# Optimization experiments

Measured on AMD Instinct MI355X. Metric: run time of the kernel, lower is better.

## Reference

```python
import jax, jax.numpy as jnp
import numpy as np

D_MODEL = 2048
NUM_HEADS = 16
D_K = D_MODEL // NUM_HEADS
THETA = 10000.0
BATCH, SEQ = 2, 2048


def setup_inputs() -> dict:
    key = jax.random.key(0)
    ks = jax.random.split(key, 5)
    scale = 1.0 / np.sqrt(D_MODEL)
    x = jax.random.normal(ks[0], (BATCH, SEQ, D_MODEL), dtype=jnp.float32)
    token_positions = jnp.broadcast_to(jnp.arange(SEQ, dtype=jnp.int32)[None, :], (BATCH, SEQ))
    Wq = jax.random.normal(ks[1], (D_MODEL, D_MODEL), dtype=jnp.float32) * scale
    Wk = jax.random.normal(ks[2], (D_MODEL, D_MODEL), dtype=jnp.float32) * scale
    Wv = jax.random.normal(ks[3], (D_MODEL, D_MODEL), dtype=jnp.float32) * scale
    Wo = jax.random.normal(ks[4], (D_MODEL, D_MODEL), dtype=jnp.float32) * scale
    return {"x": x, "token_positions": token_positions, "Wq": Wq, "Wk": Wk, "Wv": Wv, "Wo": Wo}


def _apply_rope(t, positions):
    # t: [b, h, s, d_k]; positions: [b, s]. Interleaved-pair rotation.
    half = D_K // 2
    inv_freq = THETA ** (-jnp.arange(0, half, dtype=jnp.float32) * 2.0 / D_K)  # [half]
    ang = positions.astype(jnp.float32)[:, :, None] * inv_freq[None, None, :]  # [b, s, half]
    cos = jnp.cos(ang)[:, None, :, :]  # [b, 1, s, half]
    sin = jnp.sin(ang)[:, None, :, :]
    t2 = t.reshape(*t.shape[:-1], half, 2)
    x1, x2 = t2[..., 0], t2[..., 1]
    r1 = x1 * cos - x2 * sin
    r2 = x1 * sin + x2 * cos
    return jnp.stack([r1, r2], axis=-1).reshape(t.shape)


def reference(x, token_positions, Wq, Wk, Wv, Wo):
    b, s, _ = x.shape
    # Linear layers compute x @ W^T (weight stored as [out, in], no bias)
    def proj(w):
        y = jnp.einsum('bsd,ed->bse', x, w)
        return y.reshape(b, s, NUM_HEADS, D_K).transpose(0, 2, 1, 3)  # b h s d
    Q, K, V = proj(Wq), proj(Wk), proj(Wv)
    Q = _apply_rope(Q, token_positions)
    K = _apply_rope(K, token_positions)
    scores = jnp.einsum('bhqd,bhkd->bhqk', Q, K) / jnp.sqrt(jnp.float32(D_K))
    causal = jnp.tril(jnp.ones((s, s), dtype=bool))
    scores = jnp.where(causal[None, None], scores, jnp.finfo(scores.dtype).min)
    attn = jax.nn.softmax(scores, axis=-1)
    out = jnp.einsum('bhqk,bhkd->bhqd', attn, V)  # b h s d
    out = out.transpose(0, 2, 1, 3).reshape(b, s, D_MODEL)
    return jnp.einsum('bse,de->bsd', out, Wo)
```

## Files before the change

kernel.cpp:

```cpp
#include <hip/hip_runtime.h>
#include <cstdint>
#include <cstddef>

#define D_MODEL 2048
#define NHEAD 16
#define DK 128
#define SEQ 2048
#define BATCH 2
#define NTOK (BATCH * SEQ)
#define NQB 32

typedef __bf16 bf16;
typedef __bf16 bf16x2 __attribute__((ext_vector_type(2)));
typedef __bf16 bf16x4 __attribute__((ext_vector_type(4)));
typedef __bf16 bf16x8 __attribute__((ext_vector_type(8)));
typedef float f32x4 __attribute__((ext_vector_type(4)));

__device__ __forceinline__ void g2lds16(const void* g, void* l) {
  __builtin_amdgcn_global_load_lds(
      (const __attribute__((address_space(1))) void*)g,
      (__attribute__((address_space(3))) void*)l, 16, 0, 0);
}

__device__ __forceinline__ void cstore(float* p, float v) { *p = v; }
__device__ __forceinline__ void cstore(bf16* p, float v) { *p = (bf16)v; }

#define BAR()                              \
  {                                        \
    asm volatile("" ::: "memory");         \
    __builtin_amdgcn_s_barrier();          \
    asm volatile("" ::: "memory");         \
  }

__global__ void k_f32_to_bf16(const float* __restrict__ in, bf16* __restrict__ out, int n4) {
  int i = blockIdx.x * blockDim.x + threadIdx.x;
  if (i >= n4) return;
  const float4 v = ((const float4*)in)[i];
  bf16x4 o = {(bf16)v.x, (bf16)v.y, (bf16)v.z, (bf16)v.w};
  ((bf16x4*)out)[i] = o;
}

__global__ void k_w4_to_bf16(const float* __restrict__ W0, const float* __restrict__ W1,
                             const float* __restrict__ W2, const float* __restrict__ W3,
                             bf16* __restrict__ o0, bf16* __restrict__ o1,
                             bf16* __restrict__ o2, bf16* __restrict__ o3, int n4) {
  const float* in;
  bf16* out;
  switch (blockIdx.y) {
    case 0: in = W0; out = o0; break;
    case 1: in = W1; out = o1; break;
    case 2: in = W2; out = o2; break;
    default: in = W3; out = o3;
  }
  int i = blockIdx.x * blockDim.x + threadIdx.x;
  if (i >= n4) return;
  const float4 v = ((const float4*)in)[i];
  bf16x4 o = {(bf16)v.x, (bf16)v.y, (bf16)v.z, (bf16)v.w};
  ((bf16x4*)out)[i] = o;
}

__global__ __launch_bounds__(512, 1) void k_gemm8(
    const bf16* __restrict__ A, const bf16* __restrict__ B0p, const bf16* __restrict__ B1p,
    const bf16* __restrict__ B2p, bf16* __restrict__ C0, bf16* __restrict__ C1,
    bf16* __restrict__ C2, const int* __restrict__ pos, int M, int N, int K) {
  const bf16* Bp = B0p;
  bf16* Cp = C0;
  if (blockIdx.z == 1) { Bp = B1p; Cp = C1; }
  else if (blockIdx.z == 2) { Bp = B2p; Cp = C2; }
  const bool rope = (blockIdx.z < 2);

  __shared__ bf16 Ab[2][256 * 64];
  __shared__ bf16 Bb[2][256 * 64];

  const int t = threadIdx.x;
  const int wid = t >> 6, lane = t & 63;
  const int wr = wid >> 2, wc = wid & 3;
  const int lr = lane & 15, lg = lane >> 4;
  const int bm = blockIdx.y, bn = blockIdx.x;
  const size_t arow0 = (size_t)bm * 256;
  const size_t brow0 = (size_t)bn * 256;

  const int srow = wid * 8 + (lane >> 3);
  const int schunk = ((lane & 7) ^ ((lane >> 3) & 7)) * 8;

#define STG(X, row0, k0, lb, h)                                                \
  {                                                                            \
    g2lds16(&(X)[((row0) + (h)*128 + srow) * (size_t)K + (k0) + schunk],       \
            &(lb)[((h)*128 + wid * 8) * 64]);                                  \
    g2lds16(&(X)[((row0) + (h)*128 + 64 + srow) * (size_t)K + (k0) + schunk],  \
            &(lb)[((h)*128 + 64 + wid * 8) * 64]);                             \
  }
#define LDA8(lb, mh, m, kk) \
  (*(const bf16x8*)&(lb)[((mh)*128 + wr * 64 + (m)*16 + lr) * 64 + ((((kk)*4 + lg) ^ (lr & 7)) * 8)])
#define LDB8(lb, nh, n, kk) \
  (*(const bf16x8*)&(lb)[((nh)*128 + wc * 32 + (n)*16 + lr) * 64 + ((((kk)*4 + lg) ^ (lr & 7)) * 8)])

  const int T = K >> 6;

  STG(A, arow0, 0, Ab[0], 0);
  STG(A, arow0, 0, Ab[0], 1);
  STG(Bp, brow0, 0, Bb[0], 0);
  STG(Bp, brow0, 0, Bb[0], 1);
  STG(A, arow0, 64, Ab[1], 0);

  f32x4 acc[2][2][4][2] = {};

  for (int tt = 0; tt < T; ++tt) {
    const int cur = tt & 1;
    const bf16* Ac = Ab[cur];
    const bf16* Bc = Bb[cur];
    bf16* Aw = Ab[cur];
    bf16* An = Ab[cur ^ 1];
    bf16* Bn = Bb[cur ^ 1];
    const int k1 = (tt + 1) << 6;
    const int k2 = (tt + 2) << 6;
    const bool pf1 = (tt + 1 < T);
    const bool pf2 = (tt + 2 < T);

    if (tt == T - 1) {
      asm volatile("s_waitcnt vmcnt(0)" ::: "memory");
    } else {
      asm volatile("s_waitcnt vmcnt(2)" ::: "memory");
    }
    BAR();

    bf16x8 a[4][2], b0[2][2], b1[2][2];

#pragma unroll
    for (int m = 0; m < 4; ++m)
#pragma unroll
      for (int kk = 0; kk < 2; ++kk) a[m][kk] = LDA8(Ac, 0, m, kk);
#pragma unroll
    for (int n = 0; n < 2; ++n)
#pragma unroll
      for (int kk = 0; kk < 2; ++kk) b0[n][kk] = LDB8(Bc, 0, n, kk);
    if (pf1) {
      STG(A, arow0, k1, An, 1);
      STG(Bp, brow0, k1, Bn, 0);
    }
    __builtin_amdgcn_s_setprio(1);
#pragma unroll
    for (int m = 0; m < 4; ++m)
#pragma unroll
      for (int n = 0; n < 2; ++n)
#pragma unroll
        for (int kk = 0; kk < 2; ++kk)
          acc[0][0][m][n] =
              __builtin_amdgcn_mfma_f32_16x16x32_bf16(a[m][kk], b0[n][kk], acc[0][0][m][n], 0, 0, 0);
    __builtin_amdgcn_s_setprio(0);
    BAR();

#pragma unroll
    for (int n = 0; n < 2; ++n)
#pragma unroll
      for (int kk = 0; kk < 2; ++kk) b1[n][kk] = LDB8(Bc, 1, n, kk);
    if (pf1) STG(Bp, brow0, k1, Bn, 1);
    __builtin_amdgcn_s_setprio(1);
#pragma unroll
    for (int m = 0; m < 4; ++m)
#pragma unroll
      for (int n = 0; n < 2; ++n)
#pragma unroll
        for (int kk = 0; kk < 2; ++kk)
          acc[0][1][m][n] =
              __builtin_amdgcn_mfma_f32_16x16x32_bf16(a[m][kk], b1[n][kk], acc[0][1][m][n], 0, 0, 0);
    __builtin_amdgcn_s_setprio(0);
    BAR();

#pragma unroll
    for (int m = 0; m < 4; ++m)
#pragma unroll
      for (int kk = 0; kk < 2; ++kk) a[m][kk] = LDA8(Ac, 1, m, kk);
    if (pf2) STG(A, arow0, k2, Aw, 0);
    __builtin_amdgcn_s_setprio(1);
#pragma unroll
    for (int m = 0; m < 4; ++m)
#pragma unroll
      for (int n = 0; n < 2; ++n)
#pragma unroll
        for (int kk = 0; kk < 2; ++kk)
          acc[1][1][m][n] =
              __builtin_amdgcn_mfma_f32_16x16x32_bf16(a[m][kk], b1[n][kk], acc[1][1][m][n], 0, 0, 0);
    __builtin_amdgcn_s_setprio(0);
    BAR();

    __builtin_amdgcn_s_setprio(1);
#pragma unroll
    for (int m = 0; m < 4; ++m)
#pragma unroll
      for (int n = 0; n < 2; ++n)
#pragma unroll
        for (int kk = 0; kk < 2; ++kk)
          acc[1][0][m][n] =
              __builtin_amdgcn_mfma_f32_16x16x32_bf16(a[m][kk], b0[n][kk], acc[1][0][m][n], 0, 0, 0);
    __builtin_amdgcn_s_setprio(0);
  }

  float invf[2];
#pragma unroll
  for (int n = 0; n < 2; ++n) {
    int f = ((wc * 32 + n * 16 + lr) & 127) >> 1;
    invf[n] = exp2f((float)f * -0.20762050593121503f);
  }
#pragma unroll
  for (int mh = 0; mh < 2; ++mh)
#pragma unroll
    for (int m = 0; m < 4; ++m) {
      size_t rowb = arow0 + mh * 128 + wr * 64 + m * 16 + lg * 4;
#pragma unroll
      for (int r = 0; r < 4; ++r) {
        float p = rope ? (float)pos[rowb + r] : 0.0f;
#pragma unroll
        for (int n = 0; n < 2; ++n) {
          float sn, cs;
          if (rope) __sincosf(p * invf[n], &sn, &cs);
#pragma unroll
          for (int nh = 0; nh < 2; ++nh) {
            float v = acc[mh][nh][m][n][r];
            float vp = __shfl_xor(v, 1);
            float outv = v;
            if (rope) outv = (lr & 1) ? (v * cs + vp * sn) : (v * cs - vp * sn);
            size_t col = brow0 + nh * 128 + wc * 32 + n * 16 + lr;
            Cp[(rowb + r) * N + col] = (bf16)outv;
          }
        }
      }
    }
#undef STG
#undef LDA8
#undef LDB8
}

template <typename OutT>
__global__ __launch_bounds__(256, 2) void k_gemm_nt(
    const bf16* __restrict__ A, const bf16* __restrict__ B0, const bf16* __restrict__ B1,
    const bf16* __restrict__ B2, OutT* __restrict__ C0, OutT* __restrict__ C1,
    OutT* __restrict__ C2, int M, int N, int K) {
  const bf16* Bp = B0;
  OutT* Cp = C0;
  if (blockIdx.z == 1) { Bp = B1; Cp = C1; }
  else if (blockIdx.z == 2) { Bp = B2; Cp = C2; }

  __shared__ bf16 As[128 * 32];
  __shared__ bf16 Bs[128 * 32];

  const int t = threadIdx.x;
  const int w = t >> 6;
  const int lane = t & 63;
  const int lr = lane & 15;
  const int lg = lane >> 4;
  const int wr = w >> 1, wc = w & 1;
  const int bm = blockIdx.y, bn = blockIdx.x;

  f32x4 acc[4][4] = {};

  const int srow = lane >> 2;
  const int scol = (lane & 3) * 8;

  const int kt_iters = K >> 5;
  for (int kt = 0; kt < kt_iters; ++kt) {
    const int kbase = kt * 32;
#pragma unroll
    for (int i = 0; i < 2; ++i) {
      int chunk = w * 2 + i;
      int row = chunk * 16 + srow;
      g2lds16(&A[(size_t)(bm * 128 + row) * K + kbase + scol], &As[chunk * 512]);
      g2lds16(&Bp[(size_t)(bn * 128 + row) * K + kbase + scol], &Bs[chunk * 512]);
    }
    asm volatile("s_waitcnt vmcnt(0)" ::: "memory");
    __syncthreads();

    bf16x8 af[4], bfr[4];
#pragma unroll
    for (int m = 0; m < 4; ++m)
      af[m] = *(const bf16x8*)&As[(wr * 64 + m * 16 + lr) * 32 + lg * 8];
#pragma unroll
    for (int n = 0; n < 4; ++n)
      bfr[n] = *(const bf16x8*)&Bs[(wc * 64 + n * 16 + lr) * 32 + lg * 8];
#pragma unroll
    for (int m = 0; m < 4; ++m)
#pragma unroll
      for (int n = 0; n < 4; ++n)
        acc[m][n] = __builtin_amdgcn_mfma_f32_16x16x32_bf16(af[m], bfr[n], acc[m][n], 0, 0, 0);
    __syncthreads();
  }

#pragma unroll
  for (int m = 0; m < 4; ++m) {
    int rowb = bm * 128 + wr * 64 + m * 16 + lg * 4;
#pragma unroll
    for (int n = 0; n < 4; ++n) {
      int col = bn * 128 + wc * 64 + n * 16 + lr;
#pragma unroll
      for (int r = 0; r < 4; ++r) cstore(&Cp[(size_t)(rowb + r) * N + col], acc[m][n][r]);
    }
  }
}

__global__ __launch_bounds__(256, 2) void k_attn(const bf16* __restrict__ Q,
                                                 const bf16* __restrict__ K,
                                                 const bf16* __restrict__ V,
                                                 bf16* __restrict__ O) {
  const int wg = blockIdx.x;
  const int g = wg & 7;
  const int i = wg >> 3;
  const int bh = g + 8 * (i & 3);
  const int pr = i >> 2;
  const int b = bh >> 4, h = bh & 15;

  const int t = threadIdx.x;
  const int w = t >> 6, lane = t & 63;
  const int lr = lane & 15, lg = lane >> 4;

  const size_t rowbase = (size_t)b * SEQ;
  const int hoff = h * DK;

  __shared__ bf16 Ks[2][64 * 128];
  __shared__ uint32_t VTu[2][128 * 32];
  __shared__ bf16 Pb[4][16 * 64];

  const int kp = t & 31;
  const int d0s = (t >> 5) * 16;

  const float scale = 0.08838834764831845f;
  const float FIXM = 8.0f;

  bf16x8 sa0, sa1, sb0, sb1;
  int cur = 0;

  const int krow_l = lane >> 4;
  const int kchunk = lane & 15;

  for (int qsel = 0; qsel < 2; ++qsel) {
    const int qblk = qsel ? pr : (NQB - 1 - pr);
    const int qb = qblk * 64;
    const int ktiles = qblk + 1;

    bf16x8 qf[4];
    {
      size_t qrow = rowbase + qb + w * 16 + lr;
#pragma unroll
      for (int c = 0; c < 4; ++c)
        qf[c] = *(const bf16x8*)&Q[qrow * D_MODEL + hoff + c * 32 + lg * 8];
    }

    f32x4 o[8] = {};
    f32x4 lrow = {};

#pragma unroll
    for (int j = 0; j < 4; ++j) {
      int row = w * 16 + j * 4 + krow_l;
      int chunk = kchunk ^ (j * 4 + krow_l);
      g2lds16(&K[(rowbase + row) * D_MODEL + hoff + chunk * 8],
              &Ks[cur][(size_t)(w * 16 + j * 4) * 128]);
    }
    {
      const bf16* vp0 = &V[(rowbase + 2 * kp) * D_MODEL + hoff + d0s];
      sa0 = *(const bf16x8*)vp0;
      sa1 = *(const bf16x8*)(vp0 + 8);
      sb0 = *(const bf16x8*)(vp0 + D_MODEL);
      sb1 = *(const bf16x8*)(vp0 + D_MODEL + 8);
    }

    for (int kt = 0; kt < ktiles; ++kt) {
      const int k0 = kt * 64;
#pragma unroll
      for (int j = 0; j < 8; ++j) {
        int d = d0s + j;
        bf16x2 p0 = {sa0[j], sb0[j]};
        VTu[cur][d * 32 + (kp ^ ((d & 7) << 2))] = *(const uint32_t*)&p0;
      }
#pragma unroll
      for (int j = 0; j < 8; ++j) {
        int d = d0s + 8 + j;
        bf16x2 p1 = {sa1[j], sb1[j]};
        VTu[cur][d * 32 + (kp ^ ((d & 7) << 2))] = *(const uint32_t*)&p1;
      }
      asm volatile("s_waitcnt vmcnt(0)" ::: "memory");
      __syncthreads();

      if (kt + 1 < ktiles) {
#pragma unroll
        for (int j = 0; j < 4; ++j) {
          int row = w * 16 + j * 4 + krow_l;
          int chunk = kchunk ^ (j * 4 + krow_l);
          g2lds16(&K[(rowbase + k0 + 64 + row) * D_MODEL + hoff + chunk * 8],
                  &Ks[cur ^ 1][(size_t)(w * 16 + j * 4) * 128]);
        }
        const bf16* vp0 = &V[(rowbase + k0 + 64 + 2 * kp) * D_MODEL + hoff + d0s];
        sa0 = *(const bf16x8*)vp0;
        sa1 = *(const bf16x8*)(vp0 + 8);
        sb0 = *(const bf16x8*)(vp0 + D_MODEL);
        sb1 = *(const bf16x8*)(vp0 + D_MODEL + 8);
      }

      f32x4 sc[4];
      __builtin_amdgcn_s_setprio(1);
#pragma unroll
      for (int tt = 0; tt < 4; ++tt) {
        f32x4 a = {};
#pragma unroll
        for (int c = 0; c < 4; ++c) {
          bf16x8 kf = *(const bf16x8*)&Ks[cur][(tt * 16 + lr) * 128 + (((c * 4 + lg) ^ lr) * 8)];
          a = __builtin_amdgcn_mfma_f32_16x16x32_bf16(qf[c], kf, a, 0, 0, 0);
        }
        sc[tt] = a * scale;
      }
      __builtin_amdgcn_s_setprio(0);

      const int qrow0 = qb + w * 16 + lg * 4;
      if (k0 + 64 > qb + w * 16) {
#pragma unroll
        for (int tt = 0; tt < 4; ++tt) {
          int kcol = k0 + tt * 16 + lr;
#pragma unroll
          for (int r = 0; r < 4; ++r)
            if (kcol > qrow0 + r) sc[tt][r] = -3.0e38f;
        }
      }

#pragma unroll
      for (int tt = 0; tt < 4; ++tt)
#pragma unroll
        for (int r = 0; r < 4; ++r) {
          float p = __expf(sc[tt][r] - FIXM);
          sc[tt][r] = p;
          lrow[r] += p;
        }

#pragma unroll
      for (int tt = 0; tt < 4; ++tt)
#pragma unroll
        for (int r = 0; r < 4; ++r) {
          int q = lg * 4 + r;
          int col = tt * 16 + lr;
          Pb[w][q * 64 + (col ^ ((q & 7) << 3))] = (bf16)sc[tt][r];
        }
      asm volatile("s_waitcnt lgkmcnt(0)" ::: "memory");
      bf16x8 pf0 = *(const bf16x8*)&Pb[w][lr * 64 + ((lg * 8) ^ ((lr & 7) << 3))];
      bf16x8 pf1 = *(const bf16x8*)&Pb[w][lr * 64 + ((32 + lg * 8) ^ ((lr & 7) << 3))];

      __builtin_amdgcn_s_setprio(1);
#pragma unroll
      for (int nt = 0; nt < 8; ++nt) {
        int d = nt * 16 + lr;
        bf16x8 vf0 = *(const bf16x8*)&VTu[cur][d * 32 + ((lg * 4) ^ ((d & 7) << 2))];
        bf16x8 vf1 = *(const bf16x8*)&VTu[cur][d * 32 + ((16 + lg * 4) ^ ((d & 7) << 2))];
        o[nt] = __builtin_amdgcn_mfma_f32_16x16x32_bf16(pf0, vf0, o[nt], 0, 0, 0);
        o[nt] = __builtin_amdgcn_mfma_f32_16x16x32_bf16(pf1, vf1, o[nt], 0, 0, 0);
      }
      __builtin_amdgcn_s_setprio(0);
      cur ^= 1;
    }

#pragma unroll
    for (int off = 8; off >= 1; off >>= 1)
#pragma unroll
      for (int r = 0; r < 4; ++r) lrow[r] += __shfl_xor(lrow[r], off);

    size_t orow = rowbase + qb + w * 16 + lg * 4;
#pragma unroll
    for (int nt = 0; nt < 8; ++nt)
#pragma unroll
      for (int r = 0; r < 4; ++r)
        O[(orow + r) * D_MODEL + hoff + nt * 16 + lr] = (bf16)(o[nt][r] / lrow[r]);
  }
}

extern "C" void kernel_launch(void* const* d_in, const int* in_sizes, int n_in, void* d_out,
                              int out_size, void* d_ws, size_t ws_size, hipStream_t stream) {
  const float* x = (const float*)d_in[0];
  const int* pos = (const int*)d_in[1];
  const float* Wq = (const float*)d_in[2];
  const float* Wk = (const float*)d_in[3];
  const float* Wv = (const float*)d_in[4];
  const float* Wo = (const float*)d_in[5];
  float* out = (float*)d_out;

  char* ws = (char*)d_ws;
  const size_t MB = 1u << 20;
  bf16* xb  = (bf16*)(ws);
  bf16* wqb = (bf16*)(ws + 16 * MB);
  bf16* wkb = (bf16*)(ws + 24 * MB);
  bf16* wvb = (bf16*)(ws + 32 * MB);
  bf16* wob = (bf16*)(ws + 40 * MB);
  bf16* Qb  = (bf16*)(ws + 48 * MB);
  bf16* Kb  = (bf16*)(ws + 64 * MB);
  bf16* Vb  = (bf16*)(ws + 80 * MB);
  bf16* AOb = (bf16*)(ws + 96 * MB);

  {
    int n4 = NTOK * D_MODEL / 4;
    k_f32_to_bf16<<<(n4 + 255) / 256, 256, 0, stream>>>(x, xb, n4);
    int w4 = D_MODEL * D_MODEL / 4;
    k_w4_to_bf16<<<dim3((w4 + 255) / 256, 4), 256, 0, stream>>>(
        Wq, Wk, Wv, Wo, wqb, wkb, wvb, wob, w4);
  }
  {
    dim3 g(D_MODEL / 256, NTOK / 256, 3);
    k_gemm8<<<g, 512, 0, stream>>>(xb, wqb, wkb, wvb, Qb, Kb, Vb, pos,
                                   NTOK, D_MODEL, D_MODEL);
  }
  k_attn<<<dim3(NQB * NHEAD * BATCH / 2, 1, 1), 256, 0, stream>>>(Qb, Kb, Vb, AOb);
  {
    dim3 g(D_MODEL / 128, NTOK / 128, 1);
    k_gemm_nt<float><<<g, 256, 0, stream>>>(AOb, wob, wob, wob, out, out, out, NTOK, D_MODEL, D_MODEL);
  }
}
```

Measured before the change: 262.5 us.

## Use 128-row query blocks with 8 waves in attention and merge conversion launches

The attention kernel now processes 128 query rows per block with 512 threads (8 waves), instead of 64 rows with 4 waves. Each K/V tile staged in shared memory is therefore reused by twice as many query rows, and the grid shrinks to 256 blocks. Each thread now loads half as much V data per tile. Separately, the x and weight fp32-to-bf16 conversions are merged into one 5-way launch to save a kernel launch, though the weight slices launch extra blocks that exit immediately. Fewer, larger attention blocks may reduce occupancy and worsen the balance of the causal workload.

```diff
diff --git a/kernel.cpp b/kernel.cpp
--- a/kernel.cpp
+++ b/kernel.cpp
@@ -8,7 +8,6 @@
 #define SEQ 2048
 #define BATCH 2
 #define NTOK (BATCH * SEQ)
-#define NQB 32
 
 typedef __bf16 bf16;
 typedef __bf16 bf16x2 __attribute__((ext_vector_type(2)));
@@ -32,28 +31,24 @@
     asm volatile("" ::: "memory");         \
   }
 
-__global__ void k_f32_to_bf16(const float* __restrict__ in, bf16* __restrict__ out, int n4) {
-  int i = blockIdx.x * blockDim.x + threadIdx.x;
-  if (i >= n4) return;
-  const float4 v = ((const float4*)in)[i];
-  bf16x4 o = {(bf16)v.x, (bf16)v.y, (bf16)v.z, (bf16)v.w};
-  ((bf16x4*)out)[i] = o;
-}
-
-__global__ void k_w4_to_bf16(const float* __restrict__ W0, const float* __restrict__ W1,
-                             const float* __restrict__ W2, const float* __restrict__ W3,
-                             bf16* __restrict__ o0, bf16* __restrict__ o1,
-                             bf16* __restrict__ o2, bf16* __restrict__ o3, int n4) {
+__global__ void k_conv5(const float* __restrict__ X, const float* __restrict__ W0,
+                        const float* __restrict__ W1, const float* __restrict__ W2,
+                        const float* __restrict__ W3, bf16* __restrict__ xo,
+                        bf16* __restrict__ o0, bf16* __restrict__ o1,
+                        bf16* __restrict__ o2, bf16* __restrict__ o3,
+                        int nx4, int nw4) {
   const float* in;
   bf16* out;
+  int n;
   switch (blockIdx.y) {
-    case 0: in = W0; out = o0; break;
-    case 1: in = W1; out = o1; break;
-    case 2: in = W2; out = o2; break;
-    default: in = W3; out = o3;
+    case 0: in = X; out = xo; n = nx4; break;
+    case 1: in = W0; out = o0; n = nw4; break;
+    case 2: in = W1; out = o1; n = nw4; break;
+    case 3: in = W2; out = o2; n = nw4; break;
+    default: in = W3; out = o3; n = nw4;
   }
   int i = blockIdx.x * blockDim.x + threadIdx.x;
-  if (i >= n4) return;
+  if (i >= n) return;
   const float4 v = ((const float4*)in)[i];
   bf16x4 o = {(bf16)v.x, (bf16)v.y, (bf16)v.z, (bf16)v.w};
   ((bf16x4*)out)[i] = o;
@@ -297,7 +292,7 @@
   }
 }
 
-__global__ __launch_bounds__(256, 2) void k_attn(const bf16* __restrict__ Q,
+__global__ __launch_bounds__(512, 2) void k_attn(const bf16* __restrict__ Q,
                                                  const bf16* __restrict__ K,
                                                  const bf16* __restrict__ V,
                                                  bf16* __restrict__ O) {
@@ -317,24 +312,24 @@
 
   __shared__ bf16 Ks[2][64 * 128];
   __shared__ uint32_t VTu[2][128 * 32];
-  __shared__ bf16 Pb[4][16 * 64];
+  __shared__ bf16 Pb[8][16 * 64];
 
   const int kp = t & 31;
-  const int d0s = (t >> 5) * 16;
-
+  const int d0s = (t >> 5) * 8;
+
+  const float FIXM = 8.0f;
   const float scale = 0.08838834764831845f;
-  const float FIXM = 8.0f;
-
-  bf16x8 sa0, sa1, sb0, sb1;
-  int cur = 0;
 
   const int krow_l = lane >> 4;
   const int kchunk = lane & 15;
 
+  bf16x8 sa, sb;
+  int cur = 0;
+
   for (int qsel = 0; qsel < 2; ++qsel) {
-    const int qblk = qsel ? pr : (NQB - 1 - pr);
-    const int qb = qblk * 64;
-    const int ktiles = qblk + 1;
+    const int qblk = qsel ? pr : (15 - pr);
+    const int qb = qblk * 128;
+    const int ktiles = 2 * qblk + 2;
 
     bf16x8 qf[4];
     {
@@ -348,18 +343,16 @@
     f32x4 lrow = {};
 
 #pragma unroll
-    for (int j = 0; j < 4; ++j) {
-      int row = w * 16 + j * 4 + krow_l;
-      int chunk = kchunk ^ (j * 4 + krow_l);
+    for (int j = 0; j < 2; ++j) {
+      int row = w * 8 + j * 4 + krow_l;
+      int chunk = kchunk ^ (row & 15);
       g2lds16(&K[(rowbase + row) * D_MODEL + hoff + chunk * 8],
-              &Ks[cur][(size_t)(w * 16 + j * 4) * 128]);
+              &Ks[cur][(size_t)(w * 8 + j * 4) * 128]);
     }
     {
-      const bf16* vp0 = &V[(rowbase + 2 * kp) * D_MODEL + hoff + d0s];
-      sa0 = *(const bf16x8*)vp0;
-      sa1 = *(const bf16x8*)(vp0 + 8);
-      sb0 = *(const bf16x8*)(vp0 + D_MODEL);
-      sb1 = *(const bf16x8*)(vp0 + D_MODEL + 8);
+      const bf16* vp = &V[(rowbase + 2 * kp) * D_MODEL + hoff + d0s];
+      sa = *(const bf16x8*)vp;
+      sb = *(const bf16x8*)(vp + D_MODEL);
     }
 
     for (int kt = 0; kt < ktiles; ++kt) {
@@ -367,31 +360,23 @@
 #pragma unroll
       for (int j = 0; j < 8; ++j) {
         int d = d0s + j;
-        bf16x2 p0 = {sa0[j], sb0[j]};
-        VTu[cur][d * 32 + (kp ^ ((d & 7) << 2))] = *(const uint32_t*)&p0;
-      }
-#pragma unroll
-      for (int j = 0; j < 8; ++j) {
-        int d = d0s + 8 + j;
-        bf16x2 p1 = {sa1[j], sb1[j]};
-        VTu[cur][d * 32 + (kp ^ ((d & 7) << 2))] = *(const uint32_t*)&p1;
+        bf16x2 pr2 = {sa[j], sb[j]};
+        VTu[cur][d * 32 + (kp ^ ((d & 7) << 2))] = *(const uint32_t*)&pr2;
       }
       asm volatile("s_waitcnt vmcnt(0)" ::: "memory");
       __syncthreads();
 
       if (kt + 1 < ktiles) {
 #pragma unroll
-        for (int j = 0; j < 4; ++j) {
-          int row = w * 16 + j * 4 + krow_l;
-          int chunk = kchunk ^ (j * 4 + krow_l);
+        for (int j = 0; j < 2; ++j) {
+          int row = w * 8 + j * 4 + krow_l;
+          int chunk = kchunk ^ (row & 15);
           g2lds16(&K[(rowbase + k0 + 64 + row) * D_MODEL + hoff + chunk * 8],
-                  &Ks[cur ^ 1][(size_t)(w * 16 + j * 4) * 128]);
-        }
-        const bf16* vp0 = &V[(rowbase + k0 + 64 + 2 * kp) * D_MODEL + hoff + d0s];
-        sa0 = *(const bf16x8*)vp0;
-        sa1 = *(const bf16x8*)(vp0 + 8);
-        sb0 = *(const bf16x8*)(vp0 + D_MODEL);
-        sb1 = *(const bf16x8*)(vp0 + D_MODEL + 8);
+                  &Ks[cur ^ 1][(size_t)(w * 8 + j * 4) * 128]);
+        }
+        const bf16* vp = &V[(rowbase + k0 + 64 + 2 * kp) * D_MODEL + hoff + d0s];
+        sa = *(const bf16x8*)vp;
+        sb = *(const bf16x8*)(vp + D_MODEL);
       }
 
       f32x4 sc[4];
@@ -490,18 +475,17 @@
   bf16* AOb = (bf16*)(ws + 96 * MB);
 
   {
-    int n4 = NTOK * D_MODEL / 4;
-    k_f32_to_bf16<<<(n4 + 255) / 256, 256, 0, stream>>>(x, xb, n4);
-    int w4 = D_MODEL * D_MODEL / 4;
-    k_w4_to_bf16<<<dim3((w4 + 255) / 256, 4), 256, 0, stream>>>(
-        Wq, Wk, Wv, Wo, wqb, wkb, wvb, wob, w4);
+    int nx4 = NTOK * D_MODEL / 4;
+    int nw4 = D_MODEL * D_MODEL / 4;
+    k_conv5<<<dim3((nx4 + 255) / 256, 5), 256, 0, stream>>>(
+        x, Wq, Wk, Wv, Wo, xb, wqb, wkb, wvb, wob, nx4, nw4);
   }
   {
     dim3 g(D_MODEL / 256, NTOK / 256, 3);
     k_gemm8<<<g, 512, 0, stream>>>(xb, wqb, wkb, wvb, Qb, Kb, Vb, pos,
                                    NTOK, D_MODEL, D_MODEL);
   }
-  k_attn<<<dim3(NQB * NHEAD * BATCH / 2, 1, 1), 256, 0, stream>>>(Qb, Kb, Vb, AOb);
+  k_attn<<<dim3(256, 1, 1), 512, 0, stream>>>(Qb, Kb, Vb, AOb);
   {
     dim3 g(D_MODEL / 128, NTOK / 128, 1);
     k_gemm_nt<float><<<g, 256, 0, stream>>>(AOb, wob, wob, wob, out, out, out, NTOK, D_MODEL, D_MODEL);
```

Result: slower. 270.6 us (+3.1%).
